# Optimization experiments

Hardware: AMD Instinct MI355X
Metric: run time of the kernel (lower is better)

Reference implementation:

```python
import jax, jax.numpy as jnp
import numpy as np

EMBED = 1024
HEADS = 16
HEAD_DIM = EMBED // HEADS


def setup_inputs() -> dict:
    key = jax.random.key(0)
    ks = jax.random.split(key, 12)
    B, S, D = 4, 2048, EMBED
    scale = 1.0 / np.sqrt(D)
    inp = {
        "query": jax.random.normal(ks[0], (B, S, D), dtype=jnp.float32),
        "key": jax.random.normal(ks[1], (B, S, D), dtype=jnp.float32),
        "value": jax.random.normal(ks[2], (B, S, D), dtype=jnp.float32),
        "Wq": jax.random.normal(ks[3], (D, D), dtype=jnp.float32) * scale,
        "bq": jnp.zeros((D,), dtype=jnp.float32),
        "Wk": jax.random.normal(ks[4], (D, D), dtype=jnp.float32) * scale,
        "bk": jnp.zeros((D,), dtype=jnp.float32),
        "Wv": jax.random.normal(ks[5], (D, D), dtype=jnp.float32) * scale,
        "bv": jnp.zeros((D,), dtype=jnp.float32),
        "Wo": jax.random.normal(ks[6], (D, D), dtype=jnp.float32) * scale,
        "bo": jnp.zeros((D,), dtype=jnp.float32),
    }
    return inp


def reference(query, key, value, Wq, bq, Wk, bk, Wv, bv, Wo, bo):
    B, S, D = query.shape
    H, Dh = HEADS, HEAD_DIM

    def proj(x, W, b):
        # nn.Linear: x @ W.T + b, then split heads -> [B, H, S, Dh]
        y = jnp.einsum('bsd,ed->bse', x, W) + b
        return y.reshape(B, -1, H, Dh).transpose(0, 2, 1, 3)

    q = proj(query, Wq, bq)
    k = proj(key, Wk, bk)
    v = proj(value, Wv, bv)

    attn = jnp.einsum('bhqd,bhkd->bhqk', q, k) / jnp.sqrt(jnp.float32(Dh))
    attn = jax.nn.softmax(attn, axis=-1)
    # dropout: eval mode -> identity
    out = jnp.einsum('bhqk,bhkd->bhqd', attn, v)
    out = out.transpose(0, 2, 1, 3).reshape(B, -1, D)
    out = jnp.einsum('bsd,ed->bse', out, Wo) + bo
    return out
```

## Files before the change

### kernel.cpp

```cpp
#include <hip/hip_runtime.h>
#include <hip/hip_bf16.h>

typedef unsigned short u16;
typedef unsigned int u32;
typedef float f32x4 __attribute__((ext_vector_type(4)));
typedef float f32x16 __attribute__((ext_vector_type(16)));
typedef __bf16 bf16x8 __attribute__((ext_vector_type(8)));
typedef u32 u32x2 __attribute__((ext_vector_type(2)));

#define DEV static __device__ __forceinline__

DEV u16 f2b(float f) { __bf16 h = (__bf16)f; u16 r; __builtin_memcpy(&r, &h, 2); return r; }
DEV u32 pk2(float a, float b) { return (u32)f2b(a) | ((u32)f2b(b) << 16); }
DEV bf16x8 as_bf(uint4 v) { bf16x8 r; __builtin_memcpy(&r, &v, 16); return r; }

#define GLDS(g, l) __builtin_amdgcn_global_load_lds( \
    (__attribute__((address_space(1))) void*)(g),     \
    (__attribute__((address_space(3))) void*)(l), 16, 0, 0)

DEV void wb2() { asm volatile("s_waitcnt vmcnt(2)\n\ts_barrier" ::: "memory"); }
DEV void wb4() { asm volatile("s_waitcnt vmcnt(4)\n\ts_barrier" ::: "memory"); }
DEV void wb0() { asm volatile("s_waitcnt vmcnt(0)\n\ts_barrier" ::: "memory"); }

__global__ __launch_bounds__(256) void conva_k(const float* __restrict__ src,
                                               u16* __restrict__ dst, int n8)
{
  int i = blockIdx.x * 256 + threadIdx.x;
  const int stride = gridDim.x * 256;
  for (; i < n8; i += stride) {
    const float4* p = (const float4*)(src + (size_t)i * 8);
    const float4 a = p[0], b = p[1];
    *(uint4*)(dst + (size_t)i * 8) =
        make_uint4(pk2(a.x, a.y), pk2(a.z, a.w), pk2(b.x, b.y), pk2(b.z, b.w));
  }
}

__global__ __launch_bounds__(256) void convw_k(const float* __restrict__ w0,
                                               const float* __restrict__ w1,
                                               const float* __restrict__ w2,
                                               const float* __restrict__ w3,
                                               u16* __restrict__ dst)
{
  const int seg = blockIdx.x >> 9, sb = blockIdx.x & 511;
  const float* s = seg == 0 ? w0 : seg == 1 ? w1 : seg == 2 ? w2 : w3;
  const int i = sb * 256 + threadIdx.x;
  const float4* p = (const float4*)(s + (size_t)i * 8);
  const float4 a = p[0], b = p[1];
  *(uint4*)(dst + (size_t)seg * 1048576 + (size_t)i * 8) =
      make_uint4(pk2(a.x, a.y), pk2(a.z, a.w), pk2(b.x, b.y), pk2(b.z, b.w));
}

template<int CMODE>
__global__ __launch_bounds__(256) void gemm_b(const u16* __restrict__ A,
                                              const u16* __restrict__ W,
                                              const float* __restrict__ bias,
                                              void* __restrict__ Cp, float scale)
{
  __shared__ u16 lds[3][8192];
  const int tid = threadIdx.x;
  const int lane = tid & 63, w = tid >> 6;
  const int m0 = blockIdx.x * 128, e0 = blockIdx.y * 128;
  const int wrb = (w >> 1) * 4, wcb = (w & 1) * 4;

  f32x4 acc[4][4];
#pragma unroll
  for (int i = 0; i < 4; i++)
#pragma unroll
    for (int j = 0; j < 4; j++)
#pragma unroll
      for (int r = 0; r < 4; r++) acc[i][j][r] = 0.f;

  const u16* gA = A + (size_t)(m0 + w * 32 + (lane & 15)) * 1024 + (lane >> 4) * 8;
  const u16* gB = W + (size_t)(e0 + w * 32 + (lane & 15)) * 1024 + (lane >> 4) * 8;

#define GSTAGE(K0, BUF)                                        \
  GLDS(gA + (K0),         &lds[BUF][w * 1024]);                \
  GLDS(gA + (K0) + 16384, &lds[BUF][w * 1024 + 512]);          \
  GLDS(gB + (K0),         &lds[BUF][4096 + w * 1024]);         \
  GLDS(gB + (K0) + 16384, &lds[BUF][4096 + w * 1024 + 512]);

  GSTAGE(0, 0)
  GSTAGE(32, 1)

  const int fo = (lane >> 4) * 128 + (lane & 15) * 8;

#define GEMM_STEP(BUF)                                                         \
  {                                                                            \
    const u16* la = &lds[BUF][0];                                              \
    const u16* lb = &lds[BUF][4096];                                           \
    bf16x8 af[4], bfr[4];                                                      \
    _Pragma("unroll")                                                          \
    for (int i = 0; i < 4; i++) {                                              \
      af[i]  = as_bf(*(const uint4*)(la + (wrb + i) * 512 + fo));              \
      bfr[i] = as_bf(*(const uint4*)(lb + (wcb + i) * 512 + fo));              \
    }                                                                          \
    _Pragma("unroll")                                                          \
    for (int i = 0; i < 4; i++)                                                \
      _Pragma("unroll")                                                        \
      for (int j = 0; j < 4; j++)                                              \
        acc[i][j] = __builtin_amdgcn_mfma_f32_16x16x32_bf16(af[i], bfr[j],     \
                                                            acc[i][j], 0, 0, 0); \
  }

  for (int t = 0; t < 30; t += 3) {
    wb4(); GSTAGE((t + 2) * 32, 2) GEMM_STEP(0)
    wb4(); GSTAGE((t + 3) * 32, 0) GEMM_STEP(1)
    wb4(); GSTAGE((t + 4) * 32, 1) GEMM_STEP(2)
  }
  wb4(); GEMM_STEP(0)
  wb0(); GEMM_STEP(1)
#undef GEMM_STEP
#undef GSTAGE

  const int col = lane & 15, rb4 = (lane >> 4) * 4;
  const int wr = wrb * 16, wc = wcb * 16;
#pragma unroll
  for (int j = 0; j < 4; j++) {
    const int e = e0 + wc + j * 16 + col;
    const float bv = bias[e];
#pragma unroll
    for (int i = 0; i < 4; i++) {
#pragma unroll
      for (int r = 0; r < 4; r++) {
        const int m = m0 + wr + i * 16 + rb4 + r;
        const float v = (acc[i][j][r] + bv) * scale;
        if (CMODE == 0) {
          ((float*)Cp)[(size_t)m * 1024 + e] = v;
        } else {
          const int b = m >> 11, s = m & 2047, h = e >> 6, dh = e & 63;
          const size_t bh = (size_t)(b * 16 + h);
          if (CMODE == 2) {
            const size_t idx = (((bh * 64 + (s >> 5)) * 4 + (dh >> 4)) * 64
                                + ((dh >> 3) & 1) * 32 + (s & 31)) * 8 + (dh & 7);
            ((u16*)Cp)[idx] = f2b(v);
          } else {
            const size_t idx = ((bh * 64 + (s >> 5)) * 8 + ((s >> 4) & 1) * 4
                                + (dh >> 5) * 2 + ((s >> 3) & 1)) * 256
                               + (size_t)(dh & 31) * 8 + (s & 7);
            ((u16*)Cp)[idx] = f2b(v);
          }
        }
      }
    }
  }
}

__global__ __launch_bounds__(256, 4) void attn_k(const u16* __restrict__ Qb,
                                                 const u16* __restrict__ Kb,
                                                 const u16* __restrict__ Vb,
                                                 u16* __restrict__ O)
{
  __shared__ u16 pool[12288];
  const int tid = threadIdx.x, wv = tid >> 6, lane = tid & 63;
  const int lo = lane & 31, hi = lane >> 5;
  const int bid = blockIdx.x;
  const int xcd = bid & 7, ix = bid >> 3;
  const int bh = xcd * 8 + (ix & 7);
  const int qb = (ix >> 3) * 4 + wv;
  const int b = bh >> 4, h = bh & 15, q0 = qb * 32;

  const u16* qp = Qb + ((size_t)(bh * 64 + qb) * 4) * 512 + (size_t)lane * 8;
  bf16x8 qf[4];
#pragma unroll
  for (int c = 0; c < 4; c++) qf[c] = as_bf(*(const uint4*)(qp + c * 512));

  f32x16 a0, a1, zv;
#pragma unroll
  for (int r = 0; r < 16; r++) { a0[r] = 0.f; a1[r] = 0.f; zv[r] = 0.f; }
  float ls0 = 0.f, ls1 = 0.f;

  const u16* sgK = Kb + (size_t)bh * 131072 + wv * 512 + (size_t)lane * 8;
  const u16* sgV = Vb + (size_t)bh * 131072 + wv * 512 + (size_t)lane * 8;

#define ASTAGE(T, BUF)                                                  \
  GLDS(sgK + (size_t)(T) * 2048, pool + (BUF) * 4096 + wv * 512);       \
  GLDS(sgV + (size_t)(T) * 2048, pool + (BUF) * 4096 + 2048 + wv * 512);

  ASTAGE(0, 0)
  ASTAGE(1, 1)

#define ATTN_STEP(BUF)                                                        \
  {                                                                           \
    const u16* kl = pool + (BUF) * 4096;                                      \
    const u16* vl = kl + 2048;                                                \
    __builtin_amdgcn_s_setprio(1);                                            \
    f32x16 s = __builtin_amdgcn_mfma_f32_32x32x16_bf16(                       \
                 as_bf(*(const uint4*)(kl + lane * 8)), qf[0], zv, 0, 0, 0);  \
    _Pragma("unroll")                                                         \
    for (int c = 1; c < 4; c++)                                               \
      s = __builtin_amdgcn_mfma_f32_32x32x16_bf16(                            \
            as_bf(*(const uint4*)(kl + c * 512 + lane * 8)), qf[c], s, 0, 0, 0); \
    __builtin_amdgcn_s_setprio(0);                                            \
    _Pragma("unroll")                                                         \
    for (int r = 0; r < 16; r++) s[r] = __builtin_amdgcn_exp2f(s[r]);         \
    _Pragma("unroll")                                                         \
    for (int r = 0; r < 16; r += 2) { ls0 += s[r]; ls1 += s[r + 1]; }         \
    bf16x8 pf[2];                                                             \
    _Pragma("unroll")                                                         \
    for (int kc = 0; kc < 2; kc++) {                                          \
      const u32 A0 = pk2(s[8 * kc + 0], s[8 * kc + 1]);                       \
      const u32 A1 = pk2(s[8 * kc + 2], s[8 * kc + 3]);                       \
      const u32 B0 = pk2(s[8 * kc + 4], s[8 * kc + 5]);                       \
      const u32 B1 = pk2(s[8 * kc + 6], s[8 * kc + 7]);                       \
      u32x2 w02 = __builtin_amdgcn_permlane32_swap(A0, B0, false, false);     \
      u32x2 w13 = __builtin_amdgcn_permlane32_swap(A1, B1, false, false);     \
      pf[kc] = as_bf(make_uint4(w02[0], w13[0], w02[1], w13[1]));             \
    }                                                                         \
    __builtin_amdgcn_s_setprio(1);                                            \
    a0 = __builtin_amdgcn_mfma_f32_32x32x16_bf16(                             \
           as_bf(*(const uint4*)(vl + 0    + lane * 8)), pf[0], a0, 0, 0, 0); \
    a1 = __builtin_amdgcn_mfma_f32_32x32x16_bf16(                             \
           as_bf(*(const uint4*)(vl + 512  + lane * 8)), pf[0], a1, 0, 0, 0); \
    a0 = __builtin_amdgcn_mfma_f32_32x32x16_bf16(                             \
           as_bf(*(const uint4*)(vl + 1024 + lane * 8)), pf[1], a0, 0, 0, 0); \
    a1 = __builtin_amdgcn_mfma_f32_32x32x16_bf16(                             \
           as_bf(*(const uint4*)(vl + 1536 + lane * 8)), pf[1], a1, 0, 0, 0); \
    __builtin_amdgcn_s_setprio(0);                                            \
  }

  for (int t = 0; t < 60; t += 3) {
    wb2(); ASTAGE(t + 2, 2) ATTN_STEP(0)
    wb2(); ASTAGE(t + 3, 0) ATTN_STEP(1)
    wb2(); ASTAGE(t + 4, 1) ATTN_STEP(2)
  }
  wb2(); ASTAGE(62, 2) ATTN_STEP(0)
  wb2(); ASTAGE(63, 0) ATTN_STEP(1)
  wb2(); ATTN_STEP(2)
  wb0(); ATTN_STEP(0)
#undef ATTN_STEP
#undef ASTAGE

  __syncthreads();

  float l = ls0 + ls1;
  l += __shfl_xor(l, 32);
  const float inv = 1.f / l;
  u16* ob = pool + (wv * 32) * 72;

#pragma unroll
  for (int r = 0; r < 16; r++) {
    const int dh = (r & 3) + 8 * (r >> 2) + 4 * hi;
    ob[lo * 72 + dh]      = f2b(a0[r] * inv);
    ob[lo * 72 + dh + 32] = f2b(a1[r] * inv);
  }
  __builtin_amdgcn_s_barrier();
  const int qr = lane >> 1, hf = lane & 1;
  const u16* src = ob + qr * 72 + hf * 32;
  const uint4 r0 = *(const uint4*)(src + 0);
  const uint4 r1 = *(const uint4*)(src + 8);
  const uint4 r2 = *(const uint4*)(src + 16);
  const uint4 r3 = *(const uint4*)(src + 24);
  const size_t m = (size_t)b * 2048 + q0 + qr;
  uint4* dst = (uint4*)(O + m * 1024 + (size_t)h * 64 + hf * 32);
  dst[0] = r0; dst[1] = r1; dst[2] = r2; dst[3] = r3;
}

extern "C" void kernel_launch(void* const* d_in, const int* in_sizes, int n_in,
                              void* d_out, int out_size, void* d_ws, size_t ws_size,
                              hipStream_t stream)
{
  const float* query = (const float*)d_in[0];
  const float* key   = (const float*)d_in[1];
  const float* value = (const float*)d_in[2];
  const float* Wq = (const float*)d_in[3];
  const float* bq = (const float*)d_in[4];
  const float* Wk = (const float*)d_in[5];
  const float* bk = (const float*)d_in[6];
  const float* Wv = (const float*)d_in[7];
  const float* bv = (const float*)d_in[8];
  const float* Wo = (const float*)d_in[9];
  const float* bo = (const float*)d_in[10];

  const size_t MAT = (size_t)8192 * 1024;
  const size_t WMAT = (size_t)1024 * 1024;
  if (ws_size < (4 * MAT + 4 * WMAT) * sizeof(u16)) return;
  u16* Ac = (u16*)d_ws;
  u16* Wc = Ac + MAT;
  u16* Qw = Wc + 4 * WMAT;
  u16* Kw = Qw + MAT;
  u16* Vw = Kw + MAT;
  u16* Ow = Ac;

  const float qscale = 0.125f * 1.4426950408889634f;

  dim3 bl(256, 1, 1), gg(64, 8);
  hipLaunchKernelGGL(convw_k, dim3(2048), bl, 0, stream, Wq, Wk, Wv, Wo, Wc);

  hipLaunchKernelGGL(conva_k, dim3(2048), bl, 0, stream, query, Ac, (int)(MAT / 8));
  hipLaunchKernelGGL((gemm_b<2>), gg, bl, 0, stream, Ac, Wc + 0 * WMAT, bq, (void*)Qw, qscale);

  hipLaunchKernelGGL(conva_k, dim3(2048), bl, 0, stream, key, Ac, (int)(MAT / 8));
  hipLaunchKernelGGL((gemm_b<2>), gg, bl, 0, stream, Ac, Wc + 1 * WMAT, bk, (void*)Kw, 1.0f);

  hipLaunchKernelGGL(conva_k, dim3(2048), bl, 0, stream, value, Ac, (int)(MAT / 8));
  hipLaunchKernelGGL((gemm_b<3>), gg, bl, 0, stream, Ac, Wc + 2 * WMAT, bv, (void*)Vw, 1.0f);

  hipLaunchKernelGGL(attn_k, dim3(1024), bl, 0, stream, Qw, Kw, Vw, Ow);

  hipLaunchKernelGGL((gemm_b<0>), gg, bl, 0, stream, Ow, Wc + 3 * WMAT, bo, d_out, 1.0f);
}
```

Measured before the change: 262.9 us.

## Fuse fp32-to-bf16 activation conversion into a batched QKV projection GEMM

Removes the three separate activation conversion kernels by having the QKV GEMM load fp32 activations into registers, convert them to bf16 and write them to LDS. The three projections are merged into one launch with a z-dimension of 3, which fills more of the GPU per launch. In exchange, the A-tile path moves from async global-to-LDS loads to register loads with a full vmcnt(0)/lgkmcnt(0) wait every step, which can reduce overlap inside the GEMM. The output GEMM becomes a dedicated kernel without the scale and layout branching.

```diff
diff --git a/kernel.cpp b/kernel.cpp
--- a/kernel.cpp
+++ b/kernel.cpp
@@ -18,22 +18,10 @@
     (__attribute__((address_space(1))) void*)(g),     \
     (__attribute__((address_space(3))) void*)(l), 16, 0, 0)
 
-DEV void wb2() { asm volatile("s_waitcnt vmcnt(2)\n\ts_barrier" ::: "memory"); }
-DEV void wb4() { asm volatile("s_waitcnt vmcnt(4)\n\ts_barrier" ::: "memory"); }
-DEV void wb0() { asm volatile("s_waitcnt vmcnt(0)\n\ts_barrier" ::: "memory"); }
-
-__global__ __launch_bounds__(256) void conva_k(const float* __restrict__ src,
-                                               u16* __restrict__ dst, int n8)
-{
-  int i = blockIdx.x * 256 + threadIdx.x;
-  const int stride = gridDim.x * 256;
-  for (; i < n8; i += stride) {
-    const float4* p = (const float4*)(src + (size_t)i * 8);
-    const float4 a = p[0], b = p[1];
-    *(uint4*)(dst + (size_t)i * 8) =
-        make_uint4(pk2(a.x, a.y), pk2(a.z, a.w), pk2(b.x, b.y), pk2(b.z, b.w));
-  }
-}
+DEV void wb2()  { asm volatile("s_waitcnt vmcnt(2)\n\ts_barrier" ::: "memory"); }
+DEV void wb4()  { asm volatile("s_waitcnt vmcnt(4)\n\ts_barrier" ::: "memory"); }
+DEV void wb0()  { asm volatile("s_waitcnt vmcnt(0)\n\ts_barrier" ::: "memory"); }
+DEV void wb0l() { asm volatile("s_waitcnt vmcnt(0) lgkmcnt(0)\n\ts_barrier" ::: "memory"); }
 
 __global__ __launch_bounds__(256) void convw_k(const float* __restrict__ w0,
                                                const float* __restrict__ w1,
@@ -50,18 +38,32 @@
       make_uint4(pk2(a.x, a.y), pk2(a.z, a.w), pk2(b.x, b.y), pk2(b.z, b.w));
 }
 
-template<int CMODE>
-__global__ __launch_bounds__(256) void gemm_b(const u16* __restrict__ A,
-                                              const u16* __restrict__ W,
-                                              const float* __restrict__ bias,
-                                              void* __restrict__ Cp, float scale)
+__global__ __launch_bounds__(256) void gemm_qkv(const float* __restrict__ Aq,
+                                                const float* __restrict__ Ak,
+                                                const float* __restrict__ Av,
+                                                const u16* __restrict__ Wc,
+                                                const float* __restrict__ bq,
+                                                const float* __restrict__ bk,
+                                                const float* __restrict__ bv,
+                                                u16* __restrict__ Qw,
+                                                u16* __restrict__ Kw,
+                                                u16* __restrict__ Vw,
+                                                float qscale)
 {
   __shared__ u16 lds[3][8192];
   const int tid = threadIdx.x;
   const int lane = tid & 63, w = tid >> 6;
+  const int z = blockIdx.z;
   const int m0 = blockIdx.x * 128, e0 = blockIdx.y * 128;
   const int wrb = (w >> 1) * 4, wcb = (w & 1) * 4;
 
+  const float* Af = z == 0 ? Aq : (z == 1 ? Ak : Av);
+  const u16* Wp = Wc + (size_t)z * 1048576;
+  const float* bias = z == 0 ? bq : (z == 1 ? bk : bv);
+  u16* Cp = z == 0 ? Qw : (z == 1 ? Kw : Vw);
+  const float scale = z == 0 ? qscale : 1.0f;
+  const int cmode = (z == 2) ? 3 : 2;
+
   f32x4 acc[4][4];
 #pragma unroll
   for (int i = 0; i < 4; i++)
@@ -70,17 +72,26 @@
 #pragma unroll
       for (int r = 0; r < 4; r++) acc[i][j][r] = 0.f;
 
-  const u16* gA = A + (size_t)(m0 + w * 32 + (lane & 15)) * 1024 + (lane >> 4) * 8;
-  const u16* gB = W + (size_t)(e0 + w * 32 + (lane & 15)) * 1024 + (lane >> 4) * 8;
-
-#define GSTAGE(K0, BUF)                                        \
-  GLDS(gA + (K0),         &lds[BUF][w * 1024]);                \
-  GLDS(gA + (K0) + 16384, &lds[BUF][w * 1024 + 512]);          \
+  const float* gAf = Af + (size_t)(m0 + w * 32 + (lane & 15)) * 1024 + (lane >> 4) * 8;
+  const u16*   gB  = Wp + (size_t)(e0 + w * 32 + (lane & 15)) * 1024 + (lane >> 4) * 8;
+  const int aoff = w * 1024 + (lane >> 4) * 128 + (lane & 15) * 8;
+
+  float4 fA0, fA1, fA2, fA3;
+
+#define GSB(K0, BUF)                                           \
   GLDS(gB + (K0),         &lds[BUF][4096 + w * 1024]);         \
   GLDS(gB + (K0) + 16384, &lds[BUF][4096 + w * 1024 + 512]);
 
-  GSTAGE(0, 0)
-  GSTAGE(32, 1)
+#define LOAD_A(K0)                                             \
+  { const float* s0 = gAf + (K0); const float* s1 = s0 + 16384; \
+    fA0 = ((const float4*)s0)[0]; fA1 = ((const float4*)s0)[1]; \
+    fA2 = ((const float4*)s1)[0]; fA3 = ((const float4*)s1)[1]; }
+
+#define WRITE_A(BUF)                                                          \
+  { *(uint4*)&lds[BUF][aoff] = make_uint4(pk2(fA0.x, fA0.y), pk2(fA0.z, fA0.w), \
+                                          pk2(fA1.x, fA1.y), pk2(fA1.z, fA1.w)); \
+    *(uint4*)&lds[BUF][aoff + 512] = make_uint4(pk2(fA2.x, fA2.y), pk2(fA2.z, fA2.w), \
+                                                pk2(fA3.x, fA3.y), pk2(fA3.z, fA3.w)); }
 
   const int fo = (lane >> 4) * 128 + (lane & 15) * 8;
 
@@ -102,6 +113,104 @@
                                                             acc[i][j], 0, 0, 0); \
   }
 
+  GSB(0, 0)
+  LOAD_A(0)
+  WRITE_A(0)
+  GSB(32, 1)
+  LOAD_A(32)
+
+  for (int t = 0; t < 30; t += 3) {
+    wb0l(); GSB((t + 2) * 32, 2) WRITE_A(1) LOAD_A((t + 2) * 32) GEMM_STEP(0)
+    wb0l(); GSB((t + 3) * 32, 0) WRITE_A(2) LOAD_A((t + 3) * 32) GEMM_STEP(1)
+    wb0l(); GSB((t + 4) * 32, 1) WRITE_A(0) LOAD_A((t + 4) * 32) GEMM_STEP(2)
+  }
+  wb0l(); WRITE_A(1) GEMM_STEP(0)
+  wb0l(); GEMM_STEP(1)
+#undef GEMM_STEP
+#undef WRITE_A
+#undef LOAD_A
+#undef GSB
+
+  const int col = lane & 15, rb4 = (lane >> 4) * 4;
+  const int wr = wrb * 16, wc = wcb * 16;
+#pragma unroll
+  for (int j = 0; j < 4; j++) {
+    const int e = e0 + wc + j * 16 + col;
+    const float bv2 = bias[e];
+#pragma unroll
+    for (int i = 0; i < 4; i++) {
+#pragma unroll
+      for (int r = 0; r < 4; r++) {
+        const int m = m0 + wr + i * 16 + rb4 + r;
+        const float v = (acc[i][j][r] + bv2) * scale;
+        const int b = m >> 11, s = m & 2047, h = e >> 6, dh = e & 63;
+        const size_t bh = (size_t)(b * 16 + h);
+        if (cmode == 2) {
+          const size_t idx = (((bh * 64 + (s >> 5)) * 4 + (dh >> 4)) * 64
+                              + ((dh >> 3) & 1) * 32 + (s & 31)) * 8 + (dh & 7);
+          Cp[idx] = f2b(v);
+        } else {
+          const size_t idx = ((bh * 64 + (s >> 5)) * 8 + ((s >> 4) & 1) * 4
+                              + (dh >> 5) * 2 + ((s >> 3) & 1)) * 256
+                             + (size_t)(dh & 31) * 8 + (s & 7);
+          Cp[idx] = f2b(v);
+        }
+      }
+    }
+  }
+}
+
+__global__ __launch_bounds__(256) void gemm_o(const u16* __restrict__ A,
+                                              const u16* __restrict__ W,
+                                              const float* __restrict__ bias,
+                                              float* __restrict__ Cp)
+{
+  __shared__ u16 lds[3][8192];
+  const int tid = threadIdx.x;
+  const int lane = tid & 63, w = tid >> 6;
+  const int m0 = blockIdx.x * 128, e0 = blockIdx.y * 128;
+  const int wrb = (w >> 1) * 4, wcb = (w & 1) * 4;
+
+  f32x4 acc[4][4];
+#pragma unroll
+  for (int i = 0; i < 4; i++)
+#pragma unroll
+    for (int j = 0; j < 4; j++)
+#pragma unroll
+      for (int r = 0; r < 4; r++) acc[i][j][r] = 0.f;
+
+  const u16* gA = A + (size_t)(m0 + w * 32 + (lane & 15)) * 1024 + (lane >> 4) * 8;
+  const u16* gB = W + (size_t)(e0 + w * 32 + (lane & 15)) * 1024 + (lane >> 4) * 8;
+
+#define GSTAGE(K0, BUF)                                        \
+  GLDS(gA + (K0),         &lds[BUF][w * 1024]);                \
+  GLDS(gA + (K0) + 16384, &lds[BUF][w * 1024 + 512]);          \
+  GLDS(gB + (K0),         &lds[BUF][4096 + w * 1024]);         \
+  GLDS(gB + (K0) + 16384, &lds[BUF][4096 + w * 1024 + 512]);
+
+  GSTAGE(0, 0)
+  GSTAGE(32, 1)
+
+  const int fo = (lane >> 4) * 128 + (lane & 15) * 8;
+
+#define GEMM_STEP(BUF)                                                         \
+  {                                                                            \
+    const u16* la = &lds[BUF][0];                                              \
+    const u16* lb = &lds[BUF][4096];                                           \
+    bf16x8 af[4], bfr[4];                                                      \
+    _Pragma("unroll")                                                          \
+    for (int i = 0; i < 4; i++) {                                              \
+      af[i]  = as_bf(*(const uint4*)(la + (wrb + i) * 512 + fo));              \
+      bfr[i] = as_bf(*(const uint4*)(lb + (wcb + i) * 512 + fo));              \
+    }                                                                          \
+    _Pragma("unroll")                                                          \
+    for (int i = 0; i < 4; i++)                                                \
+      _Pragma("unroll")                                                        \
+      for (int j = 0; j < 4; j++)                                              \
+        acc[i][j] = __builtin_amdgcn_mfma_f32_16x16x32_bf16(af[i], bfr[j],     \
+                                                            acc[i][j], 0, 0, 0); \
+  }
+
   for (int t = 0; t < 30; t += 3) {
     wb4(); GSTAGE((t + 2) * 32, 2) GEMM_STEP(0)
     wb4(); GSTAGE((t + 3) * 32, 0) GEMM_STEP(1)
@@ -123,23 +232,7 @@
 #pragma unroll
       for (int r = 0; r < 4; r++) {
         const int m = m0 + wr + i * 16 + rb4 + r;
-        const float v = (acc[i][j][r] + bv) * scale;
-        if (CMODE == 0) {
-          ((float*)Cp)[(size_t)m * 1024 + e] = v;
-        } else {
-          const int b = m >> 11, s = m & 2047, h = e >> 6, dh = e & 63;
-          const size_t bh = (size_t)(b * 16 + h);
-          if (CMODE == 2) {
-            const size_t idx = (((bh * 64 + (s >> 5)) * 4 + (dh >> 4)) * 64
-                                + ((dh >> 3) & 1) * 32 + (s & 31)) * 8 + (dh & 7);
-            ((u16*)Cp)[idx] = f2b(v);
-          } else {
-            const size_t idx = ((bh * 64 + (s >> 5)) * 8 + ((s >> 4) & 1) * 4
-                                + (dh >> 5) * 2 + ((s >> 3) & 1)) * 256
-                               + (size_t)(dh & 31) * 8 + (s & 7);
-            ((u16*)Cp)[idx] = f2b(v);
-          }
-        }
+        Cp[(size_t)m * 1024 + e] = acc[i][j][r] + bv;
       }
     }
   }
@@ -274,28 +367,22 @@
   const size_t MAT = (size_t)8192 * 1024;
   const size_t WMAT = (size_t)1024 * 1024;
   if (ws_size < (4 * MAT + 4 * WMAT) * sizeof(u16)) return;
-  u16* Ac = (u16*)d_ws;
-  u16* Wc = Ac + MAT;
+  u16* Wc = (u16*)d_ws;
   u16* Qw = Wc + 4 * WMAT;
   u16* Kw = Qw + MAT;
   u16* Vw = Kw + MAT;
-  u16* Ow = Ac;
+  u16* Ow = Vw + MAT;
 
   const float qscale = 0.125f * 1.4426950408889634f;
 
-  dim3 bl(256, 1, 1), gg(64, 8);
+  dim3 bl(256, 1, 1);
   hipLaunchKernelGGL(convw_k, dim3(2048), bl, 0, stream, Wq, Wk, Wv, Wo, Wc);
 
-  hipLaunchKernelGGL(conva_k, dim3(2048), bl, 0, stream, query, Ac, (int)(MAT / 8));
-  hipLaunchKernelGGL((gemm_b<2>), gg, bl, 0, stream, Ac, Wc + 0 * WMAT, bq, (void*)Qw, qscale);
-
-  hipLaunchKernelGGL(conva_k, dim3(2048), bl, 0, stream, key, Ac, (int)(MAT / 8));
-  hipLaunchKernelGGL((gemm_b<2>), gg, bl, 0, stream, Ac, Wc + 1 * WMAT, bk, (void*)Kw, 1.0f);
-
-  hipLaunchKernelGGL(conva_k, dim3(2048), bl, 0, stream, value, Ac, (int)(MAT / 8));
-  hipLaunchKernelGGL((gemm_b<3>), gg, bl, 0, stream, Ac, Wc + 2 * WMAT, bv, (void*)Vw, 1.0f);
+  hipLaunchKernelGGL(gemm_qkv, dim3(64, 8, 3), bl, 0, stream,
+                     query, key, value, Wc, bq, bk, bv, Qw, Kw, Vw, qscale);
 
   hipLaunchKernelGGL(attn_k, dim3(1024), bl, 0, stream, Qw, Kw, Vw, Ow);
 
-  hipLaunchKernelGGL((gemm_b<0>), gg, bl, 0, stream, Ow, Wc + 3 * WMAT, bo, d_out, 1.0f);
-}
+  hipLaunchKernelGGL(gemm_o, dim3(64, 8), bl, 0, stream,
+                     Ow, Wc + 3 * WMAT, bo, (float*)d_out);
+}
```

After: 295.1 us. 1.12x slower.
